# Kernel optimization log

Measured on AMD Instinct MI355X. Metric: run time of the kernel, lower is better.

The kernel has to match this reference:

```python
import jax, jax.numpy as jnp
import numpy as np

MARGIN = 0.3
HARD_FACTOR = 0.0
NO_POS = 1000000.0
BIG = jnp.finfo(jnp.float32).max


def setup_inputs() -> dict:
    key = jax.random.key(0)
    k1, k2 = jax.random.split(key)
    global_feat = jax.random.normal(k1, (4096, 256), dtype=jnp.float32)
    labels = jax.random.randint(k2, (4096,), 0, 512, dtype=jnp.int64)
    return {"global_feat": global_feat, "labels": labels}


def euclidean_dist(x, y):
    # [m, n] pairwise distances via GEMM trick, clamped before sqrt
    xx = jnp.sum(x * x, axis=1, keepdims=True)          # [m, 1]
    yy = jnp.sum(y * y, axis=1, keepdims=True).T        # [1, n]
    d2 = xx + yy - 2.0 * (x @ y.T)
    return jnp.sqrt(jnp.maximum(d2, 1e-12))


def reference(global_feat, labels):
    feat = global_feat.astype(jnp.float32)
    dist_mat = euclidean_dist(feat, feat)               # [N, N]

    is_pos = labels[None, :] == labels[:, None]         # [N, N]
    is_neg = ~is_pos

    # hardest positive: masked row max; hardest negative: masked row min
    pos_max = jnp.max(jnp.where(is_pos, dist_mat, -BIG), axis=1)
    neg_min = jnp.min(jnp.where(is_neg, dist_mat, BIG), axis=1)
    has_pos = jnp.any(is_pos, axis=1)
    has_neg = jnp.any(is_neg, axis=1)
    dist_ap = jnp.where(has_pos, pos_max, NO_POS)
    dist_an = jnp.where(has_neg, neg_min, 0.0)

    dist_ap = dist_ap * (1.0 + HARD_FACTOR)
    dist_an = dist_an * (1.0 - HARD_FACTOR)

    valid = (dist_ap < NO_POS) & (dist_an > 0)
    n_valid = jnp.sum(valid.astype(jnp.float32))

    # MarginRankingLoss(y=1): mean over valid of relu(margin + dist_ap - dist_an)
    per_elem = jnp.maximum(MARGIN + dist_ap - dist_an, 0.0)
    loss_sum = jnp.sum(jnp.where(valid, per_elem, 0.0))
    loss = jnp.where(n_valid > 0, loss_sum / jnp.maximum(n_valid, 1.0), 0.0)
    return loss
```

## Files before the change

### kernel.cpp

```cpp
#include <hip/hip_runtime.h>
#include <hip/hip_bf16.h>

#define N 4096
#define D 256
#define MARGIN 0.3f
#define FLT_MAX_BITS 0x7F7FFFFF

typedef __attribute__((ext_vector_type(8))) short short8;
typedef __attribute__((ext_vector_type(4))) float f32x4;
typedef const __attribute__((address_space(1))) unsigned char g1_t;
typedef __attribute__((address_space(3))) unsigned char l3_t;

__device__ __forceinline__ ushort f2bf(float f) {
    unsigned u = __float_as_uint(f);
    unsigned r = (u + 0x7fffu + ((u >> 16) & 1u)) >> 16;
    return (ushort)r;
}

__global__ __launch_bounds__(256) void prep_kernel(
        const float* __restrict__ feat,
        float* __restrict__ xx,
        int* __restrict__ apbits,
        int* __restrict__ anbits,
        ushort* __restrict__ hi) {
    int row  = blockIdx.x * 4 + (threadIdx.x >> 6);
    int lane = threadIdx.x & 63;
    float4 v = *(const float4*)(feat + row * D + lane * 4);
    *(ushort4*)(hi + row * D + lane * 4) =
        make_ushort4(f2bf(v.x), f2bf(v.y), f2bf(v.z), f2bf(v.w));
    float s = v.x * v.x + v.y * v.y + v.z * v.z + v.w * v.w;
    #pragma unroll
    for (int off = 32; off >= 1; off >>= 1) s += __shfl_xor(s, off);
    if (lane == 0) {
        xx[row]     = s;
        apbits[row] = 0;
        anbits[row] = FLT_MAX_BITS;
    }
}

__global__ __launch_bounds__(256, 2) void dist_mfma_kernel(
        const ushort* __restrict__ hi,
        const int* __restrict__ labels, const float* __restrict__ xx,
        int* __restrict__ apbits, int* __restrict__ anbits) {
    __shared__ __attribute__((aligned(16))) short sA[128 * 64];
    __shared__ __attribute__((aligned(16))) short sB[128 * 64];

    int t = blockIdx.x, bi = 0, rem = 32;
    while (t >= rem) { t -= rem; ++bi; --rem; }
    const int bj = bi + t;
    const int rowBase = bi * 128;
    const int colBase = bj * 128;

    const int tid  = threadIdx.x;
    const int lane = tid & 63;
    const int wid  = tid >> 6;
    const int wr   = (wid >> 1) * 64;
    const int wc   = (wid & 1) * 64;
    const int l15  = lane & 15;
    const int kq   = (lane >> 4) * 8;
    const int swz  = (lane & 7) << 3;

    f32x4 acc[4][4] = {};

    for (int kt = 0; kt < D; kt += 64) {
        #pragma unroll
        for (int i = 0; i < 4; ++i) {
            int c   = i * 256 + tid;
            int row = c >> 3;
            int kc  = ((c ^ row) & 7) * 8;
            __builtin_amdgcn_global_load_lds(
                (g1_t*)(hi + (size_t)(rowBase + row) * D + kt + kc),
                (l3_t*)(sA + c * 8), 16, 0, 0);
            __builtin_amdgcn_global_load_lds(
                (g1_t*)(hi + (size_t)(colBase + row) * D + kt + kc),
                (l3_t*)(sB + c * 8), 16, 0, 0);
        }
        __syncthreads();
        #pragma unroll
        for (int h = 0; h < 2; ++h) {
            short8 af[4], bfv[4];
            #pragma unroll
            for (int m = 0; m < 4; ++m) {
                int idx = ((wr + m * 16 + l15) << 6) + h * 32 + kq;
                af[m] = *(const short8*)(sA + (idx ^ swz));
            }
            #pragma unroll
            for (int n = 0; n < 4; ++n) {
                int idx = ((wc + n * 16 + l15) << 6) + h * 32 + kq;
                bfv[n] = *(const short8*)(sB + (idx ^ swz));
            }
            #pragma unroll
            for (int m = 0; m < 4; ++m)
                #pragma unroll
                for (int n = 0; n < 4; ++n)
                    acc[m][n] = __builtin_amdgcn_mfma_f32_16x16x32_bf16(
                        af[m], bfv[n], acc[m][n], 0, 0, 0);
        }
        __syncthreads();
    }

    float xr[4][4]; int lrow[4][4];
    #pragma unroll
    for (int m = 0; m < 4; ++m)
        #pragma unroll
        for (int j = 0; j < 4; ++j) {
            int rg = rowBase + wr + m * 16 + (lane >> 4) * 4 + j;
            xr[m][j] = xx[rg]; lrow[m][j] = labels[rg];
        }
    float xc[4]; int lcol[4];
    #pragma unroll
    for (int n = 0; n < 4; ++n) {
        int cg = colBase + wc + n * 16 + l15;
        xc[n] = xx[cg]; lcol[n] = labels[cg];
    }

    float pm2[4][4], nm2[4][4];
    float cpm[4],   cnm[4];
    #pragma unroll
    for (int m = 0; m < 4; ++m)
        #pragma unroll
        for (int j = 0; j < 4; ++j) { pm2[m][j] = 0.0f; nm2[m][j] = 3.402823466e+38f; }
    #pragma unroll
    for (int n = 0; n < 4; ++n) { cpm[n] = 0.0f; cnm[n] = 3.402823466e+38f; }

    #pragma unroll
    for (int m = 0; m < 4; ++m)
        #pragma unroll
        for (int n = 0; n < 4; ++n)
            #pragma unroll
            for (int j = 0; j < 4; ++j) {
                float d2 = fmaxf(xr[m][j] + xc[n] - 2.0f * acc[m][n][j], 0.0f);
                bool pos = (lrow[m][j] == lcol[n]);
                if (pos) {
                    pm2[m][j] = fmaxf(pm2[m][j], d2);
                    cpm[n]    = fmaxf(cpm[n],    d2);
                } else {
                    nm2[m][j] = fminf(nm2[m][j], d2);
                    cnm[n]    = fminf(cnm[n],    d2);
                }
            }

    #pragma unroll
    for (int m = 0; m < 4; ++m)
        #pragma unroll
        for (int j = 0; j < 4; ++j) {
            #pragma unroll
            for (int off = 1; off <= 8; off <<= 1) {
                pm2[m][j] = fmaxf(pm2[m][j], __shfl_xor(pm2[m][j], off));
                nm2[m][j] = fminf(nm2[m][j], __shfl_xor(nm2[m][j], off));
            }
        }
    if (l15 == 0) {
        #pragma unroll
        for (int m = 0; m < 4; ++m)
            #pragma unroll
            for (int j = 0; j < 4; ++j) {
                int rg = rowBase + wr + m * 16 + (lane >> 4) * 4 + j;
                atomicMax(apbits + rg, __float_as_int(pm2[m][j]));
                atomicMin(anbits + rg, __float_as_int(nm2[m][j]));
            }
    }

    #pragma unroll
    for (int n = 0; n < 4; ++n) {
        #pragma unroll
        for (int off = 16; off <= 32; off <<= 1) {
            cpm[n] = fmaxf(cpm[n], __shfl_xor(cpm[n], off));
            cnm[n] = fminf(cnm[n], __shfl_xor(cnm[n], off));
        }
    }
    if (lane < 16) {
        #pragma unroll
        for (int n = 0; n < 4; ++n) {
            int cg = colBase + wc + n * 16 + l15;
            atomicMax(apbits + cg, __float_as_int(cpm[n]));
            atomicMin(anbits + cg, __float_as_int(cnm[n]));
        }
    }
}

__global__ __launch_bounds__(256) void loss_kernel(
        const int* __restrict__ apbits,
        const int* __restrict__ anbits,
        float* __restrict__ out) {
    __shared__ float ssum[4], scnt[4];
    int tid = threadIdx.x;
    float sum = 0.0f, cnt = 0.0f;
    for (int i = tid; i < N; i += 256) {
        float ap = sqrtf(fmaxf(__int_as_float(apbits[i]), 1e-12f));
        float an = sqrtf(fmaxf(__int_as_float(anbits[i]), 1e-12f));
        bool valid = (ap < 1.0e6f) && (an > 0.0f);
        float per = fmaxf(MARGIN + ap - an, 0.0f);
        if (valid) { sum += per; cnt += 1.0f; }
    }
    #pragma unroll
    for (int off = 32; off >= 1; off >>= 1) {
        sum += __shfl_xor(sum, off);
        cnt += __shfl_xor(cnt, off);
    }
    int wv = tid >> 6;
    if ((tid & 63) == 0) { ssum[wv] = sum; scnt[wv] = cnt; }
    __syncthreads();
    if (tid == 0) {
        float S = ssum[0] + ssum[1] + ssum[2] + ssum[3];
        float C = scnt[0] + scnt[1] + scnt[2] + scnt[3];
        out[0] = (C > 0.0f) ? S / fmaxf(C, 1.0f) : 0.0f;
    }
}

extern "C" void kernel_launch(void* const* d_in, const int* in_sizes, int n_in,
                              void* d_out, int out_size, void* d_ws, size_t ws_size,
                              hipStream_t stream) {
    const float* feat = (const float*)d_in[0];
    const int* labels = (const int*)d_in[1];
    float* xx   = (float*)d_ws;
    int* apbits = (int*)((char*)d_ws + 16384);
    int* anbits = (int*)((char*)d_ws + 32768);
    ushort* hi  = (ushort*)((char*)d_ws + 49152);
    float* out  = (float*)d_out;

    prep_kernel<<<N / 4, 256, 0, stream>>>(feat, xx, apbits, anbits, hi);
    dist_mfma_kernel<<<528, 256, 0, stream>>>(hi, labels, xx, apbits, anbits);
    loss_kernel<<<1, 256, 0, stream>>>(apbits, anbits, out);
}
```

Measured before the change: 33.65 us.

## Double-buffer LDS tiles and replace global atomics with per-tile partial slots

```diff
diff --git a/kernel.cpp b/kernel.cpp
--- a/kernel.cpp
+++ b/kernel.cpp
@@ -4,7 +4,8 @@
 #define N 4096
 #define D 256
 #define MARGIN 0.3f
-#define FLT_MAX_BITS 0x7F7FFFFF
+#define NSLOT 33
+#define FLT_BIG 3.402823466e+38f
 
 typedef __attribute__((ext_vector_type(8))) short short8;
 typedef __attribute__((ext_vector_type(4))) float f32x4;
@@ -20,9 +21,12 @@
 __global__ __launch_bounds__(256) void prep_kernel(
         const float* __restrict__ feat,
         float* __restrict__ xx,
-        int* __restrict__ apbits,
-        int* __restrict__ anbits,
-        ushort* __restrict__ hi) {
+        ushort* __restrict__ hi,
+        float* __restrict__ gacc,
+        unsigned* __restrict__ ticket) {
+    if (blockIdx.x == 0 && threadIdx.x == 0) {
+        gacc[0] = 0.0f; gacc[1] = 0.0f; *ticket = 0u;
+    }
     int row  = blockIdx.x * 4 + (threadIdx.x >> 6);
     int lane = threadIdx.x & 63;
     float4 v = *(const float4*)(feat + row * D + lane * 4);
@@ -31,19 +35,16 @@
     float s = v.x * v.x + v.y * v.y + v.z * v.z + v.w * v.w;
     #pragma unroll
     for (int off = 32; off >= 1; off >>= 1) s += __shfl_xor(s, off);
-    if (lane == 0) {
-        xx[row]     = s;
-        apbits[row] = 0;
-        anbits[row] = FLT_MAX_BITS;
-    }
+    if (lane == 0) xx[row] = s;
 }
 
 __global__ __launch_bounds__(256, 2) void dist_mfma_kernel(
         const ushort* __restrict__ hi,
         const int* __restrict__ labels, const float* __restrict__ xx,
-        int* __restrict__ apbits, int* __restrict__ anbits) {
-    __shared__ __attribute__((aligned(16))) short sA[128 * 64];
-    __shared__ __attribute__((aligned(16))) short sB[128 * 64];
+        float* __restrict__ pPart, float* __restrict__ nPart) {
+    __shared__ __attribute__((aligned(16))) short sA[2][128 * 64];
+    __shared__ __attribute__((aligned(16))) short sB[2][128 * 64];
+    __shared__ float rp[4][64], rn[4][64], cp[4][64], cn[4][64];
 
     int t = blockIdx.x, bi = 0, rem = 32;
     while (t >= rem) { t -= rem; ++bi; --rem; }
@@ -62,7 +63,7 @@
 
     f32x4 acc[4][4] = {};
 
-    for (int kt = 0; kt < D; kt += 64) {
+    auto stage = [&](int b, int kt) {
         #pragma unroll
         for (int i = 0; i < 4; ++i) {
             int c   = i * 256 + tid;
@@ -70,24 +71,30 @@
             int kc  = ((c ^ row) & 7) * 8;
             __builtin_amdgcn_global_load_lds(
                 (g1_t*)(hi + (size_t)(rowBase + row) * D + kt + kc),
-                (l3_t*)(sA + c * 8), 16, 0, 0);
+                (l3_t*)(&sA[b][c * 8]), 16, 0, 0);
             __builtin_amdgcn_global_load_lds(
                 (g1_t*)(hi + (size_t)(colBase + row) * D + kt + kc),
-                (l3_t*)(sB + c * 8), 16, 0, 0);
-        }
-        __syncthreads();
+                (l3_t*)(&sB[b][c * 8]), 16, 0, 0);
+        }
+    };
+
+    stage(0, 0);
+    __syncthreads();
+    int cur = 0;
+    for (int step = 0; step < 4; ++step) {
+        if (step < 3) stage(cur ^ 1, (step + 1) * 64);
         #pragma unroll
         for (int h = 0; h < 2; ++h) {
             short8 af[4], bfv[4];
             #pragma unroll
             for (int m = 0; m < 4; ++m) {
                 int idx = ((wr + m * 16 + l15) << 6) + h * 32 + kq;
-                af[m] = *(const short8*)(sA + (idx ^ swz));
+                af[m] = *(const short8*)(&sA[cur][idx ^ swz]);
             }
             #pragma unroll
             for (int n = 0; n < 4; ++n) {
                 int idx = ((wc + n * 16 + l15) << 6) + h * 32 + kq;
-                bfv[n] = *(const short8*)(sB + (idx ^ swz));
+                bfv[n] = *(const short8*)(&sB[cur][idx ^ swz]);
             }
             #pragma unroll
             for (int m = 0; m < 4; ++m)
@@ -97,6 +104,7 @@
                         af[m], bfv[n], acc[m][n], 0, 0, 0);
         }
         __syncthreads();
+        cur ^= 1;
     }
 
     float xr[4][4]; int lrow[4][4];
@@ -119,9 +127,9 @@
     #pragma unroll
     for (int m = 0; m < 4; ++m)
         #pragma unroll
-        for (int j = 0; j < 4; ++j) { pm2[m][j] = 0.0f; nm2[m][j] = 3.402823466e+38f; }
-    #pragma unroll
-    for (int n = 0; n < 4; ++n) { cpm[n] = 0.0f; cnm[n] = 3.402823466e+38f; }
+        for (int j = 0; j < 4; ++j) { pm2[m][j] = 0.0f; nm2[m][j] = FLT_BIG; }
+    #pragma unroll
+    for (int n = 0; n < 4; ++n) { cpm[n] = 0.0f; cnm[n] = FLT_BIG; }
 
     #pragma unroll
     for (int m = 0; m < 4; ++m)
@@ -150,17 +158,6 @@
                 nm2[m][j] = fminf(nm2[m][j], __shfl_xor(nm2[m][j], off));
             }
         }
-    if (l15 == 0) {
-        #pragma unroll
-        for (int m = 0; m < 4; ++m)
-            #pragma unroll
-            for (int j = 0; j < 4; ++j) {
-                int rg = rowBase + wr + m * 16 + (lane >> 4) * 4 + j;
-                atomicMax(apbits + rg, __float_as_int(pm2[m][j]));
-                atomicMin(anbits + rg, __float_as_int(nm2[m][j]));
-            }
-    }
-
     #pragma unroll
     for (int n = 0; n < 4; ++n) {
         #pragma unroll
@@ -169,42 +166,77 @@
             cnm[n] = fminf(cnm[n], __shfl_xor(cnm[n], off));
         }
     }
+
+    if (l15 == 0) {
+        #pragma unroll
+        for (int m = 0; m < 4; ++m)
+            #pragma unroll
+            for (int j = 0; j < 4; ++j) {
+                int r = m * 16 + (lane >> 4) * 4 + j;
+                rp[wid][r] = pm2[m][j]; rn[wid][r] = nm2[m][j];
+            }
+    }
     if (lane < 16) {
         #pragma unroll
         for (int n = 0; n < 4; ++n) {
-            int cg = colBase + wc + n * 16 + l15;
-            atomicMax(apbits + cg, __float_as_int(cpm[n]));
-            atomicMin(anbits + cg, __float_as_int(cnm[n]));
-        }
-    }
-}
-
-__global__ __launch_bounds__(256) void loss_kernel(
-        const int* __restrict__ apbits,
-        const int* __restrict__ anbits,
+            int c = n * 16 + l15;
+            cp[wid][c] = cpm[n]; cn[wid][c] = cnm[n];
+        }
+    }
+    __syncthreads();
+
+    if (tid < 128) {
+        int half = tid >> 6, r = tid & 63;
+        float p = fmaxf(rp[2 * half][r], rp[2 * half + 1][r]);
+        float q = fminf(rn[2 * half][r], rn[2 * half + 1][r]);
+        pPart[(size_t)(bj + 1) * N + rowBase + tid] = p;
+        nPart[(size_t)(bj + 1) * N + rowBase + tid] = q;
+    } else {
+        int tc = tid - 128, half = tc >> 6, c = tc & 63;
+        float p = fmaxf(cp[half][c], cp[half + 2][c]);
+        float q = fminf(cn[half][c], cn[half + 2][c]);
+        pPart[(size_t)bi * N + colBase + tc] = p;
+        nPart[(size_t)bi * N + colBase + tc] = q;
+    }
+}
+
+__global__ __launch_bounds__(256) void merge_kernel(
+        const float* __restrict__ pPart, const float* __restrict__ nPart,
+        float* __restrict__ gacc, unsigned* __restrict__ ticket,
         float* __restrict__ out) {
     __shared__ float ssum[4], scnt[4];
-    int tid = threadIdx.x;
-    float sum = 0.0f, cnt = 0.0f;
-    for (int i = tid; i < N; i += 256) {
-        float ap = sqrtf(fmaxf(__int_as_float(apbits[i]), 1e-12f));
-        float an = sqrtf(fmaxf(__int_as_float(anbits[i]), 1e-12f));
-        bool valid = (ap < 1.0e6f) && (an > 0.0f);
-        float per = fmaxf(MARGIN + ap - an, 0.0f);
-        if (valid) { sum += per; cnt += 1.0f; }
-    }
+    int i = blockIdx.x * 256 + threadIdx.x;
+    float ap2 = 0.0f, an2 = FLT_BIG;
+    #pragma unroll 3
+    for (int s = 0; s < NSLOT; ++s) {
+        ap2 = fmaxf(ap2, pPart[(size_t)s * N + i]);
+        an2 = fminf(an2, nPart[(size_t)s * N + i]);
+    }
+    float ap = sqrtf(fmaxf(ap2, 1e-12f));
+    float an = sqrtf(fmaxf(an2, 1e-12f));
+    bool valid = (ap < 1.0e6f) && (an > 0.0f);
+    float per = valid ? fmaxf(MARGIN + ap - an, 0.0f) : 0.0f;
+    float cnt = valid ? 1.0f : 0.0f;
     #pragma unroll
     for (int off = 32; off >= 1; off >>= 1) {
-        sum += __shfl_xor(sum, off);
+        per += __shfl_xor(per, off);
         cnt += __shfl_xor(cnt, off);
     }
-    int wv = tid >> 6;
-    if ((tid & 63) == 0) { ssum[wv] = sum; scnt[wv] = cnt; }
+    int tid = threadIdx.x, wv = tid >> 6;
+    if ((tid & 63) == 0) { ssum[wv] = per; scnt[wv] = cnt; }
     __syncthreads();
     if (tid == 0) {
         float S = ssum[0] + ssum[1] + ssum[2] + ssum[3];
         float C = scnt[0] + scnt[1] + scnt[2] + scnt[3];
-        out[0] = (C > 0.0f) ? S / fmaxf(C, 1.0f) : 0.0f;
+        atomicAdd(&gacc[0], S);
+        atomicAdd(&gacc[1], C);
+        __threadfence();
+        unsigned tk = atomicAdd(ticket, 1u);
+        if (tk == gridDim.x - 1) {
+            float St = atomicAdd(&gacc[0], 0.0f);
+            float Ct = atomicAdd(&gacc[1], 0.0f);
+            out[0] = (Ct > 0.0f) ? St / fmaxf(Ct, 1.0f) : 0.0f;
+        }
     }
 }
 
@@ -213,13 +245,17 @@
                               hipStream_t stream) {
     const float* feat = (const float*)d_in[0];
     const int* labels = (const int*)d_in[1];
-    float* xx   = (float*)d_ws;
-    int* apbits = (int*)((char*)d_ws + 16384);
-    int* anbits = (int*)((char*)d_ws + 32768);
-    ushort* hi  = (ushort*)((char*)d_ws + 49152);
-    float* out  = (float*)d_out;
-
-    prep_kernel<<<N / 4, 256, 0, stream>>>(feat, xx, apbits, anbits, hi);
-    dist_mfma_kernel<<<528, 256, 0, stream>>>(hi, labels, xx, apbits, anbits);
-    loss_kernel<<<1, 256, 0, stream>>>(apbits, anbits, out);
-}
+    char* ws = (char*)d_ws;
+    float*    xx     = (float*)ws;
+    float*    gacc   = (float*)(ws + 16384);
+    unsigned* ticket = (unsigned*)(ws + 16384 + 8);
+    ushort*   hi     = (ushort*)(ws + 32768);
+    float*    pPart  = (float*)(ws + 32768 + (size_t)N * D * 2);
+    float*    nPart  = (float*)(ws + 32768 + (size_t)N * D * 2
+                                + (size_t)NSLOT * N * 4);
+    float* out = (float*)d_out;
+
+    prep_kernel<<<N / 4, 256, 0, stream>>>(feat, xx, hi, gacc, ticket);
+    dist_mfma_kernel<<<528, 256, 0, stream>>>(hi, labels, xx, pPart, nPart);
+    merge_kernel<<<N / 256, 256, 0, stream>>>(pPart, nPart, gacc, ticket, out);
+}
```

Measured after the change: 37.18 us. 1.11x slower.
